# Kernel optimization log

Hardware: AMD Instinct MI355X
Metric: run time of the kernel (lower is better)

Reference implementation:

```python
import jax, jax.numpy as jnp
import numpy as np

B, T, V = 32, 100, 20000
E, H, M, DD = 128, 128, 64, 2


def setup_inputs() -> dict:
    key = jax.random.key(0)
    ks = jax.random.split(key, 12)
    x = jax.random.uniform(ks[0], (B, T, V), dtype=jnp.float32)
    # zero out trailing timesteps per example so Masking layer matters
    lens = jax.random.randint(ks[1], (B,), T * 3 // 4, T + 1)
    tmask = (jnp.arange(T)[None, :] < lens[:, None]).astype(jnp.float32)
    x = x * tmask[:, :, None]
    a = jax.random.uniform(ks[2], (B, V), dtype=jnp.float32)
    d = jax.random.normal(ks[3], (B, DD), dtype=jnp.float32)
    # parameters
    emb = jax.random.uniform(ks[4], (V, E), minval=-0.1, maxval=0.1, dtype=jnp.float32)
    s = 1.0 / np.sqrt(E)
    gru_k = jax.random.uniform(ks[5], (E, 3 * H), minval=-s, maxval=s, dtype=jnp.float32)
    gru_rk = jax.random.normal(ks[6], (H, 3 * H), dtype=jnp.float32) / np.sqrt(H)
    gru_b_i = jnp.zeros((3 * H,), jnp.float32)   # input bias (reset_after=True)
    gru_b_r = jnp.zeros((3 * H,), jnp.float32)   # recurrent bias
    s1 = 1.0 / np.sqrt(H + E)
    W1 = jax.random.uniform(ks[7], (H + E, M), minval=-s1, maxval=s1, dtype=jnp.float32)
    b1 = jnp.zeros((M,), jnp.float32)
    s2 = 1.0 / np.sqrt(M + DD)
    W2 = jax.random.uniform(ks[8], (M + DD, 1), minval=-s2, maxval=s2, dtype=jnp.float32)
    b2 = jnp.zeros((1,), jnp.float32)
    return dict(x=x, a=a, d=d, emb=emb, gru_k=gru_k, gru_rk=gru_rk,
                gru_b_i=gru_b_i, gru_b_r=gru_b_r, W1=W1, b1=b1, W2=W2, b2=b2)


def _gru_final_state(xe, mask, gru_k, gru_rk, gru_b_i, gru_b_r):
    # xe: [B,T,E], mask: [B,T] bool. Keras GRU, reset_after=True, eval mode (dropout off).
    Hn = gru_rk.shape[0]
    x_proj = jnp.einsum('bte,eh->bth', xe, gru_k) + gru_b_i  # [B,T,3H]

    def step(h, inp):
        xp_t, m_t = inp                      # [B,3H], [B]
        rec = h @ gru_rk + gru_b_r           # [B,3H]
        xz, xr, xh = jnp.split(xp_t, 3, axis=-1)
        rz, rr, rh = jnp.split(rec, 3, axis=-1)
        z = jax.nn.sigmoid(xz + rz)
        r = jax.nn.sigmoid(xr + rr)
        hh = jnp.tanh(xh + r * rh)
        h_new = z * h + (1.0 - z) * hh
        h = jnp.where(m_t[:, None], h_new, h)  # masked steps carry state
        return h, None

    h0 = jnp.zeros((xe.shape[0], Hn), xe.dtype)
    h_final, _ = jax.lax.scan(step, h0, (jnp.swapaxes(x_proj, 0, 1), jnp.swapaxes(mask, 0, 1)))
    return h_final


def reference(x, a, d, emb, gru_k, gru_rk, gru_b_i, gru_b_r, W1, b1, W2, b2):
    ae = jnp.tanh(a @ emb)                       # [B,E]
    xe = jnp.tanh(jnp.einsum('btv,ve->bte', x, emb))  # [B,T,E]
    mask = jnp.any(xe != 0.0, axis=-1)           # Masking(mask_value=0.0)
    h = _gru_final_state(xe, mask, gru_k, gru_rk, gru_b_i, gru_b_r)  # [B,H]
    c = jnp.tanh(jnp.concatenate([h, ae], axis=1) @ W1 + b1)         # [B,M]
    out = jax.nn.sigmoid(jnp.concatenate([c, d], axis=1) @ W2 + b2)  # [B,1]
    return out
```

## Files before the change

kernel.cpp:

```cpp
#include <hip/hip_runtime.h>

typedef __attribute__((ext_vector_type(8))) short short8;
typedef __attribute__((ext_vector_type(4))) float float4v;
typedef __attribute__((ext_vector_type(2))) float float2v;

#define V_ 20000

__device__ __forceinline__ unsigned short f2bf(float f) {
    union { float f; unsigned int u; } v; v.f = f;
    unsigned int u = v.u;
    u += 0x7fffu + ((u >> 16) & 1u);
    return (unsigned short)(u >> 16);
}

__device__ __forceinline__ float fast_tanh(float x) {
    float xc = fminf(15.f, fmaxf(-15.f, x));
    float e = __expf(2.f * xc);
    return (e - 1.f) / (e + 1.f);
}

__device__ __forceinline__ float sigmoidf_(float x) {
    float xc = fminf(30.f, fmaxf(-30.f, x));
    return 1.f / (1.f + __expf(-xc));
}

#define GLL16(gp, lp) __builtin_amdgcn_global_load_lds( \
    (const __attribute__((address_space(1))) void*)(gp), \
    (__attribute__((address_space(3))) void*)(lp), 16, 0, 0)

__global__ __launch_bounds__(256) void cvt_embT(const float* __restrict__ emb,
                                                unsigned short* __restrict__ embT) {
    __shared__ unsigned short tile[128 * 65];
    int tid = threadIdx.x;
    int k0 = blockIdx.x * 64;
    const float4v* e4 = (const float4v*)emb;
    #pragma unroll
    for (int c = 0; c < 8; ++c) {
        int l4 = c * 256 + tid;
        int k = l4 >> 5;
        int n4 = l4 & 31;
        float4v f = {0.f, 0.f, 0.f, 0.f};
        if (k0 + k < V_) f = e4[(size_t)(k0 + k) * 32 + n4];
        tile[(n4 * 4 + 0) * 65 + k] = f2bf(f.x);
        tile[(n4 * 4 + 1) * 65 + k] = f2bf(f.y);
        tile[(n4 * 4 + 2) * 65 + k] = f2bf(f.z);
        tile[(n4 * 4 + 3) * 65 + k] = f2bf(f.w);
    }
    __syncthreads();
    #pragma unroll
    for (int c = 0; c < 4; ++c) {
        int l8 = c * 256 + tid;
        int n = l8 >> 3, seg = l8 & 7;
        int kk = k0 + seg * 8;
        if (kk < V_) {
            short8 v;
            #pragma unroll
            for (int i = 0; i < 8; ++i) v[i] = (short)tile[n * 65 + seg * 8 + i];
            *(short8*)(embT + (size_t)n * V_ + kk) = v;
        }
    }
}

__global__ __launch_bounds__(256, 4) void big_gemm(const float* __restrict__ x,
                                                   const float* __restrict__ a,
                                                   const unsigned short* __restrict__ embT,
                                                   float* __restrict__ partial,
                                                   int ks) {
    __shared__ unsigned short Alds[2][128 * 40];
    __shared__ unsigned short Blds[2][128 * 32];
    int tid = threadIdx.x;
    int bx = blockIdx.x, by = blockIdx.y;
    int m0 = bx * 128;
    int per = 625 / ks, extra = 625 % ks;
    int kb0 = by * per + (by < extra ? by : extra);
    int nkb = per + (by < extra ? 1 : 0);

    int lane = tid & 63, wave = tid >> 6;
    int wr = wave >> 1, wc = wave & 1;
    int ln = lane & 15, quad = lane >> 4;

    float4v acc[4][4];
    #pragma unroll
    for (int i = 0; i < 4; ++i)
        #pragma unroll
        for (int j = 0; j < 4; ++j) acc[i][j] = (float4v){0.f, 0.f, 0.f, 0.f};

    int row = tid >> 1, seg = tid & 1;
    int rg = m0 + row;
    int aidx = rg - 3200; aidx = aidx < 0 ? 0 : (aidx > 31 ? 31 : aidx);
    const float* __restrict__ srcA = (rg < 3200) ? (x + (size_t)rg * V_)
                                                 : (a + (size_t)aidx * V_);
    int brow0 = tid >> 2, bkq = tid & 3;
    int wbase = tid & ~63;
    const unsigned short* gB0 = embT + (size_t)brow0 * V_ + bkq * 8;
    const unsigned short* gB1 = embT + (size_t)(64 + brow0) * V_ + bkq * 8;

    float4v fa0, fa1, fa2, fa3;

    {
        int k0 = kb0 * 32;
        const float4v* ap = (const float4v*)(srcA + k0 + seg * 16);
        fa0 = ap[0]; fa1 = ap[1]; fa2 = ap[2]; fa3 = ap[3];
        GLL16(gB0 + k0, &Blds[0][(size_t)wbase * 8]);
        GLL16(gB1 + k0, &Blds[0][(size_t)(256 + wbase) * 8]);
        short8 w0, w1;
        w0[0]=(short)f2bf(fa0.x); w0[1]=(short)f2bf(fa0.y); w0[2]=(short)f2bf(fa0.z); w0[3]=(short)f2bf(fa0.w);
        w0[4]=(short)f2bf(fa1.x); w0[5]=(short)f2bf(fa1.y); w0[6]=(short)f2bf(fa1.z); w0[7]=(short)f2bf(fa1.w);
        w1[0]=(short)f2bf(fa2.x); w1[1]=(short)f2bf(fa2.y); w1[2]=(short)f2bf(fa2.z); w1[3]=(short)f2bf(fa2.w);
        w1[4]=(short)f2bf(fa3.x); w1[5]=(short)f2bf(fa3.y); w1[6]=(short)f2bf(fa3.z); w1[7]=(short)f2bf(fa3.w);
        *(short8*)&Alds[0][row * 40 + seg * 16]     = w0;
        *(short8*)&Alds[0][row * 40 + seg * 16 + 8] = w1;
    }
    __syncthreads();

    for (int it = 0; it < nkb; ++it) {
        int buf = it & 1, nxt = buf ^ 1;
        bool more = (it + 1 < nkb);
        if (more) {
            int k0 = (kb0 + it + 1) * 32;
            const float4v* ap = (const float4v*)(srcA + k0 + seg * 16);
            fa0 = ap[0]; fa1 = ap[1]; fa2 = ap[2]; fa3 = ap[3];
            GLL16(gB0 + k0, &Blds[nxt][(size_t)wbase * 8]);
            GLL16(gB1 + k0, &Blds[nxt][(size_t)(256 + wbase) * 8]);
        }
        short8 af[4];
        #pragma unroll
        for (int i = 0; i < 4; ++i)
            af[i] = *(const short8*)&Alds[buf][(wr * 64 + i * 16 + ln) * 40 + quad * 8];
        #pragma unroll
        for (int j = 0; j < 4; ++j) {
            short8 bf = *(const short8*)&Blds[buf][(wc * 64 + j * 16 + ln) * 32 + quad * 8];
            #pragma unroll
            for (int i = 0; i < 4; ++i)
                acc[i][j] = __builtin_amdgcn_mfma_f32_16x16x32_bf16(af[i], bf, acc[i][j], 0, 0, 0);
        }
        if (more) {
            short8 w0, w1;
            w0[0]=(short)f2bf(fa0.x); w0[1]=(short)f2bf(fa0.y); w0[2]=(short)f2bf(fa0.z); w0[3]=(short)f2bf(fa0.w);
            w0[4]=(short)f2bf(fa1.x); w0[5]=(short)f2bf(fa1.y); w0[6]=(short)f2bf(fa1.z); w0[7]=(short)f2bf(fa1.w);
            w1[0]=(short)f2bf(fa2.x); w1[1]=(short)f2bf(fa2.y); w1[2]=(short)f2bf(fa2.z); w1[3]=(short)f2bf(fa2.w);
            w1[4]=(short)f2bf(fa3.x); w1[5]=(short)f2bf(fa3.y); w1[6]=(short)f2bf(fa3.z); w1[7]=(short)f2bf(fa3.w);
            *(short8*)&Alds[nxt][row * 40 + seg * 16]     = w0;
            *(short8*)&Alds[nxt][row * 40 + seg * 16 + 8] = w1;
        }
        __syncthreads();
    }

    float* dst = partial + (size_t)by * 3328 * 128;
    #pragma unroll
    for (int i = 0; i < 4; ++i) {
        #pragma unroll
        for (int j = 0; j < 4; ++j) {
            int rowb = m0 + wr * 64 + i * 16 + quad * 4;
            int col = wc * 64 + j * 16 + ln;
            #pragma unroll
            for (int r = 0; r < 4; ++r)
                dst[(size_t)(rowb + r) * 128 + col] = acc[i][j][r];
        }
    }
}

__global__ __launch_bounds__(384) void xproj_fused(const float* __restrict__ partial,
                                                   const float* __restrict__ gru_k,
                                                   const float* __restrict__ b_i,
                                                   float* __restrict__ xproj,
                                                   float* __restrict__ maskg,
                                                   float* __restrict__ ae,
                                                   int ks) {
    const size_t SL = (size_t)3328 * 128;
    int tid = threadIdx.x;
    if (blockIdx.x == 200) {
        for (int i = tid; i < 32 * 128; i += 384) {
            float s = 0.f;
            for (int k = 0; k < ks; ++k) s += partial[(size_t)k * SL + 3200 * 128 + i];
            ae[i] = fast_tanh(s);
        }
        return;
    }
    __shared__ float xs[16 * 128];
    __shared__ int anyr[16];
    int row0 = blockIdx.x * 16;
    if (tid < 16) anyr[tid] = 0;
    __syncthreads();
    const float4v* p4 = (const float4v*)partial + (size_t)row0 * 32;
    const size_t SL4 = SL / 4;
    for (int i4 = tid; i4 < 512; i4 += 384) {
        float4v s = p4[i4];
        for (int k = 1; k < ks; ++k) {
            float4v t = p4[(size_t)k * SL4 + i4];
            s.x += t.x; s.y += t.y; s.z += t.z; s.w += t.w;
        }
        float4v v;
        v.x = fast_tanh(s.x); v.y = fast_tanh(s.y);
        v.z = fast_tanh(s.z); v.w = fast_tanh(s.w);
        *(float4v*)&xs[i4 * 4] = v;
        if (v.x != 0.f || v.y != 0.f || v.z != 0.f || v.w != 0.f)
            anyr[i4 >> 5] = 1;
    }
    __syncthreads();
    if (tid < 16) maskg[row0 + tid] = anyr[tid] ? 1.f : 0.f;

    int j = tid;
    float2v acc[16];
    #pragma unroll
    for (int r = 0; r < 16; ++r) acc[r] = (float2v){0.f, 0.f};
    float bi = b_i[j];
    for (int k4 = 0; k4 < 32; ++k4) {
        float2v g01 = { gru_k[(k4 * 4 + 0) * 384 + j], gru_k[(k4 * 4 + 1) * 384 + j] };
        float2v g23 = { gru_k[(k4 * 4 + 2) * 384 + j], gru_k[(k4 * 4 + 3) * 384 + j] };
        #pragma unroll
        for (int r = 0; r < 16; ++r) {
            float4v xv = *(const float4v*)&xs[r * 128 + k4 * 4];
            float2v x01 = {xv.x, xv.y}, x23 = {xv.z, xv.w};
            acc[r] = __builtin_elementwise_fma(x01, g01, acc[r]);
            acc[r] = __builtin_elementwise_fma(x23, g23, acc[r]);
        }
    }
    #pragma unroll
    for (int r = 0; r < 16; ++r)
        xproj[(size_t)(row0 + r) * 384 + j] = (acc[r].x + acc[r].y) + bi;
}

__global__ __launch_bounds__(384) void gru_fused(const float* __restrict__ xproj,
                                                 const float* __restrict__ maskg,
                                                 const float* __restrict__ gru_rk,
                                                 const float* __restrict__ b_r,
                                                 const float* __restrict__ ae,
                                                 const float* __restrict__ d,
                                                 const float* __restrict__ W1,
                                                 const float* __restrict__ b1,
                                                 const float* __restrict__ W2,
                                                 const float* __restrict__ b2,
                                                 float* __restrict__ out) {
    int b = blockIdx.x;
    int j = threadIdx.x;
    float2v wv[64];
    #pragma unroll
    for (int i = 0; i < 64; ++i) {
        wv[i] = (float2v){ gru_rk[(2 * i) * 384 + j], gru_rk[(2 * i + 1) * 384 + j] };
    }
    float br = b_r[j];
    __shared__ float4v hs4[32];
    __shared__ float recs[384];
    __shared__ int ntS;
    float* hs = (float*)hs4;
    float hreg = 0.f;
    if (j == 0) ntS = 0;
    if (j < 128) hs[j] = 0.f;
    const float* xp_base = xproj + (size_t)b * 100 * 384;
    const float* mk = maskg + b * 100;
    float xz = 0.f, xr = 0.f, xh = 0.f;
    if (j < 128) { xz = xp_base[j]; xr = xp_base[128 + j]; xh = xp_base[256 + j]; }
    __syncthreads();
    if (j < 100 && mk[j] != 0.f) atomicMax(&ntS, j + 1);
    __syncthreads();
    int nt = ntS;
    for (int t = 0; t < nt; ++t) {
        float nxz = 0.f, nxr = 0.f, nxh = 0.f;
        if (t + 1 < nt && j < 128) {
            const float* nb = xp_base + (t + 1) * 384;
            nxz = nb[j]; nxr = nb[128 + j]; nxh = nb[256 + j];
        }
        float2v a0 = {0.f, 0.f}, a1 = {0.f, 0.f}, a2 = {0.f, 0.f}, a3 = {0.f, 0.f};
        #pragma unroll
        for (int k4 = 0; k4 < 32; k4 += 2) {
            float4v hA = hs4[k4], hB = hs4[k4 + 1];
            float2v hA0 = {hA.x, hA.y}, hA1 = {hA.z, hA.w};
            float2v hB0 = {hB.x, hB.y}, hB1 = {hB.z, hB.w};
            a0 = __builtin_elementwise_fma(hA0, wv[2 * k4 + 0], a0);
            a1 = __builtin_elementwise_fma(hA1, wv[2 * k4 + 1], a1);
            a2 = __builtin_elementwise_fma(hB0, wv[2 * k4 + 2], a2);
            a3 = __builtin_elementwise_fma(hB1, wv[2 * k4 + 3], a3);
        }
        recs[j] = br + (((a0.x + a0.y) + (a1.x + a1.y)) + ((a2.x + a2.y) + (a3.x + a3.y)));
        __syncthreads();
        if (j < 128) {
            float z = sigmoidf_(xz + recs[j]);
            float r = sigmoidf_(xr + recs[128 + j]);
            float hh = fast_tanh(xh + r * recs[256 + j]);
            float hn = z * hreg + (1.f - z) * hh;
            hreg = (mk[t] != 0.f) ? hn : hreg;
            hs[j] = hreg;
        }
        __syncthreads();
        xz = nxz; xr = nxr; xh = nxh;
    }
    if (j < 64) {
        int m = j;
        float s = b1[m];
        const float* ab = ae + b * 128;
        #pragma unroll 4
        for (int k = 0; k < 128; ++k) s = fmaf(hs[k], W1[k * 64 + m], s);
        #pragma unroll 4
        for (int k = 0; k < 128; ++k) s = fmaf(ab[k], W1[(128 + k) * 64 + m], s);
        float c = fast_tanh(s);
        float p = c * W2[m];
        #pragma unroll
        for (int off = 32; off > 0; off >>= 1) p += __shfl_down(p, off);
        if (m == 0) {
            p += d[b * 2 + 0] * W2[64] + d[b * 2 + 1] * W2[65] + b2[0];
            out[b] = sigmoidf_(p);
        }
    }
}

extern "C" void kernel_launch(void* const* d_in, const int* in_sizes, int n_in,
                              void* d_out, int out_size, void* d_ws, size_t ws_size,
                              hipStream_t stream) {
    (void)in_sizes; (void)n_in; (void)out_size;
    const float* x      = (const float*)d_in[0];
    const float* a      = (const float*)d_in[1];
    const float* d      = (const float*)d_in[2];
    const float* emb    = (const float*)d_in[3];
    const float* gru_k  = (const float*)d_in[4];
    const float* gru_rk = (const float*)d_in[5];
    const float* gbi    = (const float*)d_in[6];
    const float* gbr    = (const float*)d_in[7];
    const float* W1     = (const float*)d_in[8];
    const float* b1     = (const float*)d_in[9];
    const float* W2     = (const float*)d_in[10];
    const float* b2     = (const float*)d_in[11];
    float* out = (float*)d_out;

    char* ws = (char*)d_ws;
    unsigned short* embT = (unsigned short*)(ws);
    const size_t slice = (size_t)3328 * 128 * 4;
    float* partial = (float*)(ws + 5120000);

    int ks = 16;
    {
        size_t fixed_rest = 16384 + 12800 + 4915200;
        while (ks > 1 && 5120000 + (size_t)ks * slice + fixed_rest > ws_size) ks >>= 1;
    }
    char* after = ws + 5120000 + (size_t)ks * slice;
    float* ae      = (float*)(after);
    float* maskg   = (float*)(after + 16384);
    float* xproj   = (float*)(after + 29184);

    hipLaunchKernelGGL(cvt_embT,    dim3(313),    dim3(256), 0, stream, emb, embT);
    hipLaunchKernelGGL(big_gemm,    dim3(26, ks), dim3(256), 0, stream, x, a, embT, partial, ks);
    hipLaunchKernelGGL(xproj_fused, dim3(201),    dim3(384), 0, stream, partial, gru_k, gbi, xproj, maskg, ae, ks);
    hipLaunchKernelGGL(gru_fused,   dim3(32),     dim3(384), 0, stream, xproj, maskg, gru_rk, gbr,
                       ae, d, W1, b1, W2, b2, out);
}
```

Measured before the change: 543.3 us.

## Halve GEMM M-tile, reduce split-K, and prefetch GRU weights into L2

The big embedding GEMM now uses 64-row M tiles, giving twice as many blocks along M, and the split-K factor drops from 16 to 8. This keeps the grid size about the same while halving the partial-sum slices that xproj_fused must reduce. xproj_fused also gets 16 extra blocks that just touch gru_rk and W1 so they are warm in cache before the recurrent GRU kernel runs. Smaller tiles cut per-block reuse of the embedding tile, and each block now runs twice as many K iterations.

```diff
diff --git a/kernel.cpp b/kernel.cpp
--- a/kernel.cpp
+++ b/kernel.cpp
@@ -66,11 +66,11 @@
                                                    const unsigned short* __restrict__ embT,
                                                    float* __restrict__ partial,
                                                    int ks) {
-    __shared__ unsigned short Alds[2][128 * 40];
+    __shared__ unsigned short Alds[2][64 * 40];
     __shared__ unsigned short Blds[2][128 * 32];
     int tid = threadIdx.x;
     int bx = blockIdx.x, by = blockIdx.y;
-    int m0 = bx * 128;
+    int m0 = bx * 64;
     int per = 625 / ks, extra = 625 % ks;
     int kb0 = by * per + (by < extra ? by : extra);
     int nkb = per + (by < extra ? 1 : 0);
@@ -79,13 +79,13 @@
     int wr = wave >> 1, wc = wave & 1;
     int ln = lane & 15, quad = lane >> 4;
 
-    float4v acc[4][4];
-    #pragma unroll
-    for (int i = 0; i < 4; ++i)
+    float4v acc[2][4];
+    #pragma unroll
+    for (int i = 0; i < 2; ++i)
         #pragma unroll
         for (int j = 0; j < 4; ++j) acc[i][j] = (float4v){0.f, 0.f, 0.f, 0.f};
 
-    int row = tid >> 1, seg = tid & 1;
+    int row = tid >> 2, kseg = tid & 3;
     int rg = m0 + row;
     int aidx = rg - 3200; aidx = aidx < 0 ? 0 : (aidx > 31 ? 31 : aidx);
     const float* __restrict__ srcA = (rg < 3200) ? (x + (size_t)rg * V_)
@@ -95,21 +95,18 @@
     const unsigned short* gB0 = embT + (size_t)brow0 * V_ + bkq * 8;
     const unsigned short* gB1 = embT + (size_t)(64 + brow0) * V_ + bkq * 8;
 
-    float4v fa0, fa1, fa2, fa3;
+    float4v fa0, fa1;
 
     {
         int k0 = kb0 * 32;
-        const float4v* ap = (const float4v*)(srcA + k0 + seg * 16);
-        fa0 = ap[0]; fa1 = ap[1]; fa2 = ap[2]; fa3 = ap[3];
+        const float4v* ap = (const float4v*)(srcA + k0 + kseg * 8);
+        fa0 = ap[0]; fa1 = ap[1];
         GLL16(gB0 + k0, &Blds[0][(size_t)wbase * 8]);
         GLL16(gB1 + k0, &Blds[0][(size_t)(256 + wbase) * 8]);
-        short8 w0, w1;
+        short8 w0;
         w0[0]=(short)f2bf(fa0.x); w0[1]=(short)f2bf(fa0.y); w0[2]=(short)f2bf(fa0.z); w0[3]=(short)f2bf(fa0.w);
         w0[4]=(short)f2bf(fa1.x); w0[5]=(short)f2bf(fa1.y); w0[6]=(short)f2bf(fa1.z); w0[7]=(short)f2bf(fa1.w);
-        w1[0]=(short)f2bf(fa2.x); w1[1]=(short)f2bf(fa2.y); w1[2]=(short)f2bf(fa2.z); w1[3]=(short)f2bf(fa2.w);
-        w1[4]=(short)f2bf(fa3.x); w1[5]=(short)f2bf(fa3.y); w1[6]=(short)f2bf(fa3.z); w1[7]=(short)f2bf(fa3.w);
-        *(short8*)&Alds[0][row * 40 + seg * 16]     = w0;
-        *(short8*)&Alds[0][row * 40 + seg * 16 + 8] = w1;
+        *(short8*)&Alds[0][row * 40 + kseg * 8] = w0;
     }
     __syncthreads();
 
@@ -118,40 +115,37 @@
         bool more = (it + 1 < nkb);
         if (more) {
             int k0 = (kb0 + it + 1) * 32;
-            const float4v* ap = (const float4v*)(srcA + k0 + seg * 16);
-            fa0 = ap[0]; fa1 = ap[1]; fa2 = ap[2]; fa3 = ap[3];
+            const float4v* ap = (const float4v*)(srcA + k0 + kseg * 8);
+            fa0 = ap[0]; fa1 = ap[1];
             GLL16(gB0 + k0, &Blds[nxt][(size_t)wbase * 8]);
             GLL16(gB1 + k0, &Blds[nxt][(size_t)(256 + wbase) * 8]);
         }
-        short8 af[4];
-        #pragma unroll
-        for (int i = 0; i < 4; ++i)
-            af[i] = *(const short8*)&Alds[buf][(wr * 64 + i * 16 + ln) * 40 + quad * 8];
+        short8 af[2];
+        #pragma unroll
+        for (int i = 0; i < 2; ++i)
+            af[i] = *(const short8*)&Alds[buf][(wr * 32 + i * 16 + ln) * 40 + quad * 8];
         #pragma unroll
         for (int j = 0; j < 4; ++j) {
             short8 bf = *(const short8*)&Blds[buf][(wc * 64 + j * 16 + ln) * 32 + quad * 8];
             #pragma unroll
-            for (int i = 0; i < 4; ++i)
+            for (int i = 0; i < 2; ++i)
                 acc[i][j] = __builtin_amdgcn_mfma_f32_16x16x32_bf16(af[i], bf, acc[i][j], 0, 0, 0);
         }
         if (more) {
-            short8 w0, w1;
+            short8 w0;
             w0[0]=(short)f2bf(fa0.x); w0[1]=(short)f2bf(fa0.y); w0[2]=(short)f2bf(fa0.z); w0[3]=(short)f2bf(fa0.w);
             w0[4]=(short)f2bf(fa1.x); w0[5]=(short)f2bf(fa1.y); w0[6]=(short)f2bf(fa1.z); w0[7]=(short)f2bf(fa1.w);
-            w1[0]=(short)f2bf(fa2.x); w1[1]=(short)f2bf(fa2.y); w1[2]=(short)f2bf(fa2.z); w1[3]=(short)f2bf(fa2.w);
-            w1[4]=(short)f2bf(fa3.x); w1[5]=(short)f2bf(fa3.y); w1[6]=(short)f2bf(fa3.z); w1[7]=(short)f2bf(fa3.w);
-            *(short8*)&Alds[nxt][row * 40 + seg * 16]     = w0;
-            *(short8*)&Alds[nxt][row * 40 + seg * 16 + 8] = w1;
+            *(short8*)&Alds[nxt][row * 40 + kseg * 8] = w0;
         }
         __syncthreads();
     }
 
     float* dst = partial + (size_t)by * 3328 * 128;
     #pragma unroll
-    for (int i = 0; i < 4; ++i) {
+    for (int i = 0; i < 2; ++i) {
         #pragma unroll
         for (int j = 0; j < 4; ++j) {
-            int rowb = m0 + wr * 64 + i * 16 + quad * 4;
+            int rowb = m0 + wr * 32 + i * 16 + quad * 4;
             int col = wc * 64 + j * 16 + ln;
             #pragma unroll
             for (int r = 0; r < 4; ++r)
@@ -163,12 +157,25 @@
 __global__ __launch_bounds__(384) void xproj_fused(const float* __restrict__ partial,
                                                    const float* __restrict__ gru_k,
                                                    const float* __restrict__ b_i,
+                                                   const float* __restrict__ gru_rk,
+                                                   const float* __restrict__ W1,
                                                    float* __restrict__ xproj,
                                                    float* __restrict__ maskg,
                                                    float* __restrict__ ae,
                                                    int ks) {
     const size_t SL = (size_t)3328 * 128;
     int tid = threadIdx.x;
+    if (blockIdx.x > 200) {
+        int pb = blockIdx.x - 201;
+        int idx = pb * 384 + tid;
+        const float4v* rk4 = (const float4v*)gru_rk;
+        float4v v1 = rk4[idx];
+        float4v v2 = rk4[idx + 6144];
+        float s = v1.x + v2.x;
+        if (idx < 2080) { float4v v3 = ((const float4v*)W1)[idx]; s += v3.x; }
+        asm volatile("" :: "v"(s));
+        return;
+    }
     if (blockIdx.x == 200) {
         for (int i = tid; i < 32 * 128; i += 384) {
             float s = 0.f;
@@ -327,7 +334,7 @@
     const size_t slice = (size_t)3328 * 128 * 4;
     float* partial = (float*)(ws + 5120000);
 
-    int ks = 16;
+    int ks = 8;
     {
         size_t fixed_rest = 16384 + 12800 + 4915200;
         while (ks > 1 && 5120000 + (size_t)ks * slice + fixed_rest > ws_size) ks >>= 1;
@@ -338,8 +345,9 @@
     float* xproj   = (float*)(after + 29184);
 
     hipLaunchKernelGGL(cvt_embT,    dim3(313),    dim3(256), 0, stream, emb, embT);
-    hipLaunchKernelGGL(big_gemm,    dim3(26, ks), dim3(256), 0, stream, x, a, embT, partial, ks);
-    hipLaunchKernelGGL(xproj_fused, dim3(201),    dim3(384), 0, stream, partial, gru_k, gbi, xproj, maskg, ae, ks);
+    hipLaunchKernelGGL(big_gemm,    dim3(52, ks), dim3(256), 0, stream, x, a, embT, partial, ks);
+    hipLaunchKernelGGL(xproj_fused, dim3(217),    dim3(384), 0, stream, partial, gru_k, gbi,
+                       gru_rk, W1, xproj, maskg, ae, ks);
     hipLaunchKernelGGL(gru_fused,   dim3(32),     dim3(384), 0, stream, xproj, maskg, gru_rk, gbr,
                        ae, d, W1, b1, W2, b2, out);
 }
```

Measured after the change: 531.9 us. -2.1%, faster.
